# Optimization experiments

Measured on AMD Instinct MI355X. Metric: run time of the kernel, lower is better.

Reference implementation:

```python
import jax, jax.numpy as jnp
import numpy as np

COMMITMENT_COST = 0.25
DECAY = 0.99
EPSILON = 1e-05
NUM_EMBEDDINGS = 1024
EMBEDDING_DIM = 256


def setup_inputs() -> dict:
    key = jax.random.key(0)
    k1, k2, k3 = jax.random.split(key, 3)
    B, T, D, K = 32, 1024, EMBEDDING_DIM, NUM_EMBEDDINGS
    z = jax.random.normal(k1, (B, T, D), dtype=jnp.float32)
    # torch init is uniform(-1/K, 1/K); scaled normal is fine for a numeric reference
    embedding = jax.random.uniform(k2, (K, D), dtype=jnp.float32, minval=-1.0 / K, maxval=1.0 / K)
    ema_cluster_size = jnp.ones((K,), dtype=jnp.float32)
    ema_w = embedding.copy()
    return {"z": z, "embedding": embedding, "ema_cluster_size": ema_cluster_size, "ema_w": ema_w}


def reference(z, embedding, ema_cluster_size, ema_w):
    B, T, D = z.shape
    K = embedding.shape[0]
    flat_z = z.reshape(-1, D)                         # [N, D]
    # squared L2 distances: ||z||^2 + ||e||^2 - 2 z.e   -> [N, K]
    distances = (jnp.sum(flat_z * flat_z, axis=1, keepdims=True)
                 + jnp.sum(embedding * embedding, axis=1)
                 - 2.0 * flat_z @ embedding.T)
    encoding_indices = jnp.argmin(distances, axis=1)  # [N]
    quantized = embedding[encoding_indices].reshape(B, T, D)

    # EMA codebook update (training branch; buffers, no grad)
    cluster_counts = jax.ops.segment_sum(jnp.ones_like(encoding_indices, dtype=jnp.float32),
                                         encoding_indices, num_segments=K)
    new_cluster_size = ema_cluster_size * DECAY + (1.0 - DECAY) * cluster_counts
    n = jnp.sum(new_cluster_size)
    new_cluster_size = (new_cluster_size + EPSILON) / (n + K * EPSILON) * n
    dw = jax.ops.segment_sum(flat_z, encoding_indices, num_segments=K)  # [K, D]
    new_ema_w = ema_w * DECAY + (1.0 - DECAY) * dw
    new_embedding = new_ema_w / new_cluster_size[:, None]

    commitment_loss = jnp.mean((z - jax.lax.stop_gradient(quantized)) ** 2)
    loss = COMMITMENT_COST * commitment_loss
    # straight-through estimator
    quantized_st = z + jax.lax.stop_gradient(quantized - z)
    return (quantized_st, loss, encoding_indices.reshape(B, T),
            new_cluster_size, new_ema_w, new_embedding)
```

## Files before the change

kernel.cpp:

```cpp
#include <hip/hip_runtime.h>
#include <hip/hip_fp16.h>
#include <math.h>

#define COMMITMENT_COST 0.25f
#define DECAY 0.99f
#define EPSILON 1e-05f
#define KCODES 1024
#define DIM 256
#define NTOK 32768

#define O_QUANT 0
#define O_LOSS  8388608
#define O_IDX   8388609
#define O_CS    8421377
#define O_EMAW  8422401
#define O_EMB   8684545

#define SE_IDX    0
#define SE_ESQ    32768
#define SE_ZSQ    33792
#define SE_HIST   66560
#define SE_NM     67584
#define SE_NOVF   67585
#define SE_MLIST  67586
#define SE_OVF    100354
#define SE_OFFS   133122
#define SE_CUR    134147
#define SE_TLIST  135171
#define SE_LPART  167939

#define SQ_ZH    0
#define SQ_EH    4194304
#define SQ_MG    4325376
#define SQ_CC    4358144
#define SQ_CAND  4390912

#define THETA_F 2e-3f
#define CAND_CAP 16
#define EPSC 2e-4f

typedef __attribute__((ext_vector_type(8))) _Float16 f16x8;
typedef __attribute__((ext_vector_type(4))) float f32x4;

__global__ void pre_kernel(const float* __restrict__ z, const float* __restrict__ E,
                           float* __restrict__ zsq, float* __restrict__ esq,
                           int* __restrict__ hist, float* __restrict__ loss,
                           unsigned short* __restrict__ zh,
                           unsigned short* __restrict__ eh,
                           int* __restrict__ nm, int* __restrict__ novf) {
    const int b = blockIdx.x;
    const int wave = threadIdx.x >> 6;
    const int lane = threadIdx.x & 63;
    if (b < NTOK / 4) {
        int token = b * 4 + wave;
        float4 v = ((const float4*)(z + (size_t)token * DIM))[lane];
        ushort4 h;
        h.x = __half_as_ushort(__float2half(v.x));
        h.y = __half_as_ushort(__float2half(v.y));
        h.z = __half_as_ushort(__float2half(v.z));
        h.w = __half_as_ushort(__float2half(v.w));
        *(ushort4*)(zh + (size_t)token * DIM + lane * 4) = h;
        float s = v.x * v.x + v.y * v.y + v.z * v.z + v.w * v.w;
        #pragma unroll
        for (int off = 32; off > 0; off >>= 1) s += __shfl_down(s, off);
        if (lane == 0) zsq[token] = s;
        if (b == 0 && threadIdx.x == 4) loss[0] = 0.0f;
        if (b == 0 && threadIdx.x == 5) { *nm = 0; *novf = 0; }
    } else {
        int eb = b - NTOK / 4;
        int k = eb * 4 + wave;
        float4 v = ((const float4*)(E + (size_t)k * DIM))[lane];
        ushort4 h;
        h.x = __half_as_ushort(__float2half(v.x));
        h.y = __half_as_ushort(__float2half(v.y));
        h.z = __half_as_ushort(__float2half(v.z));
        h.w = __half_as_ushort(__float2half(v.w));
        *(ushort4*)(eh + (size_t)k * DIM + lane * 4) = h;
        float s = v.x * v.x + v.y * v.y + v.z * v.z + v.w * v.w;
        #pragma unroll
        for (int off = 32; off > 0; off >>= 1) s += __shfl_down(s, off);
        if (lane == 0) esq[k] = s;
        if (threadIdx.x < 4) hist[eb * 4 + threadIdx.x] = 0;
    }
}

__global__ __launch_bounds__(256) void dist_mfma_kernel(
        const unsigned short* __restrict__ zh, const unsigned short* __restrict__ eh,
        const float* __restrict__ esq,
        float* __restrict__ Mg, int* __restrict__ ccount,
        unsigned long long* __restrict__ cand) {
    __shared__ unsigned short Als[64 * 260];
    __shared__ unsigned short Bls[2][256 * 36];
    __shared__ float scr[64][4];
    __shared__ float runmin[64];
    __shared__ int lcnt[64];

    const int tid = threadIdx.x;
    const int wn = tid >> 6;
    const int lane = tid & 63;
    const int l15 = lane & 15, l4 = lane >> 4;
    const int tok0 = blockIdx.x * 64;

    #pragma unroll
    for (int q = 0; q < 8; ++q) {
        int c = tid + 256 * q;
        int row = c >> 5, ch = c & 31;
        *(f16x8*)(Als + row * 260 + ch * 8) =
            *(const f16x8*)(zh + (size_t)(tok0 + row) * 256 + ch * 8);
    }
    if (tid < 64) { runmin[tid] = 3.4e38f; lcnt[tid] = 0; }

    const int brow = tid >> 2, bch = tid & 3;

    #pragma unroll
    for (int q = 0; q < 4; ++q) {
        f16x8 r = *(const f16x8*)(eh + (size_t)(brow + 64 * q) * 256 + bch * 8);
        *(f16x8*)(Bls[0] + (brow + 64 * q) * 36 + bch * 8) = r;
    }
    __syncthreads();

    int cur = 0;
    for (int c0 = 0; c0 < KCODES; c0 += 256) {
        f32x4 acc[4][4];
        #pragma unroll
        for (int i = 0; i < 4; ++i)
            #pragma unroll
            for (int j = 0; j < 4; ++j)
                acc[i][j] = (f32x4){0.f, 0.f, 0.f, 0.f};

        for (int kt = 0; kt < 8; ++kt) {
            int nc0 = c0, nkt = kt + 1;
            if (nkt == 8) { nkt = 0; nc0 += 256; }
            const bool hasnext = (nc0 < KCODES);
            f16x8 rn[4];
            if (hasnext) {
                #pragma unroll
                for (int q = 0; q < 4; ++q)
                    rn[q] = *(const f16x8*)(
                        eh + (size_t)(nc0 + brow + 64 * q) * 256 + nkt * 32 + bch * 8);
            }
            f16x8 av[4], bv[4];
            #pragma unroll
            for (int i = 0; i < 4; ++i)
                av[i] = *(const f16x8*)(Als + (i * 16 + l15) * 260 + kt * 32 + l4 * 8);
            #pragma unroll
            for (int j = 0; j < 4; ++j)
                bv[j] = *(const f16x8*)(Bls[cur] + (wn * 64 + j * 16 + l15) * 36 + l4 * 8);
            #pragma unroll
            for (int i = 0; i < 4; ++i)
                #pragma unroll
                for (int j = 0; j < 4; ++j)
                    acc[i][j] = __builtin_amdgcn_mfma_f32_16x16x32_f16(
                        av[i], bv[j], acc[i][j], 0, 0, 0);
            if (hasnext) {
                #pragma unroll
                for (int q = 0; q < 4; ++q)
                    *(f16x8*)(Bls[cur ^ 1] + (brow + 64 * q) * 36 + bch * 8) = rn[q];
            }
            __syncthreads();
            cur ^= 1;
        }

        float sq[4];
        #pragma unroll
        for (int j = 0; j < 4; ++j) sq[j] = esq[c0 + wn * 64 + j * 16 + l15];

        #pragma unroll
        for (int i = 0; i < 4; ++i) {
            #pragma unroll
            for (int r = 0; r < 4; ++r) {
                float v = fminf(fminf(sq[0] - 2.0f * acc[i][0][r],
                                      sq[1] - 2.0f * acc[i][1][r]),
                                fminf(sq[2] - 2.0f * acc[i][2][r],
                                      sq[3] - 2.0f * acc[i][3][r]));
                #pragma unroll
                for (int m = 1; m < 16; m <<= 1)
                    v = fminf(v, __shfl_xor(v, m));
                if (l15 == 0) scr[i * 16 + l4 * 4 + r][wn] = v;
            }
        }
        __syncthreads();
        if (tid < 64) {
            float m = fminf(fminf(scr[tid][0], scr[tid][1]),
                            fminf(scr[tid][2], scr[tid][3]));
            runmin[tid] = fminf(runmin[tid], m);
        }
        __syncthreads();
        #pragma unroll
        for (int i = 0; i < 4; ++i) {
            #pragma unroll
            for (int r = 0; r < 4; ++r) {
                const int row = i * 16 + l4 * 4 + r;
                const float thr = runmin[row] + THETA_F;
                #pragma unroll
                for (int j = 0; j < 4; ++j) {
                    float d = sq[j] - 2.0f * acc[i][j][r];
                    if (d <= thr) {
                        int slot = atomicAdd(&lcnt[row], 1);
                        if (slot < CAND_CAP)
                            cand[(size_t)slot * NTOK + tok0 + row] =
                                (((unsigned long long)__float_as_uint(d)) << 32) |
                                (unsigned)(c0 + wn * 64 + j * 16 + l15);
                    }
                }
            }
        }
    }
    __syncthreads();
    if (tid < 64) {
        Mg[tok0 + tid] = runmin[tid];
        ccount[tok0 + tid] = lcnt[tid];
    }
}

__global__ __launch_bounds__(256) void recheck_a_kernel(
        const float* __restrict__ Mg, const int* __restrict__ ccount,
        const unsigned long long* __restrict__ cand,
        unsigned int* __restrict__ idx,
        int* __restrict__ mlist, int* __restrict__ nm,
        int* __restrict__ ovf, int* __restrict__ novf) {
    __shared__ int ps[256];
    __shared__ int base_m, base_o;
    const int tid = threadIdx.x;
    const int token = blockIdx.x * 256 + tid;
    const int cnt = ccount[token];
    const float thr = Mg[token] + THETA_F;

    const bool isovf_cap = (cnt > CAND_CAP);
    int nsurv = 0;
    int firstcode = 0;
    if (!isovf_cap) {
        for (int s = 0; s < cnt; ++s) {
            unsigned long long e = cand[(size_t)s * NTOK + token];
            float dt = __uint_as_float((unsigned)(e >> 32));
            if (dt <= thr) {
                ++nsurv;
                if (nsurv == 1) firstcode = (int)(unsigned)(e & 0x3FFull);
            }
        }
    }
    const bool ismulti = !isovf_cap && nsurv >= 2 && nsurv <= 8;
    const bool isovf = isovf_cap || (!isovf_cap && (nsurv == 0 || nsurv > 8));
    const int want = (ismulti ? 1 : 0) | ((isovf ? 1 : 0) << 16);

    ps[tid] = want;
    __syncthreads();
    #pragma unroll
    for (int off = 1; off < 256; off <<= 1) {
        int v = (tid >= off) ? ps[tid - off] : 0;
        __syncthreads();
        ps[tid] += v;
        __syncthreads();
    }
    if (tid == 255) {
        int tot = ps[255];
        base_m = (tot & 0xFFFF) ? atomicAdd(nm, tot & 0xFFFF) : 0;
        base_o = (tot >> 16) ? atomicAdd(novf, tot >> 16) : 0;
    }
    __syncthreads();
    const int off_m = (ps[tid] - want) & 0xFFFF;
    const int off_o = (ps[tid] - want) >> 16;

    if (!isovf_cap && nsurv == 1) idx[token] = (unsigned)firstcode;
    if (ismulti) mlist[base_m + off_m] = token;
    if (isovf)   ovf[base_o + off_o] = token;
}

#define RB_BLOCKS 1024
__global__ __launch_bounds__(256) void recheck_b_kernel(
        const float* __restrict__ z, const float* __restrict__ E,
        const float* __restrict__ zsq, const float* __restrict__ esq,
        const float* __restrict__ Mg, const int* __restrict__ ccount,
        const unsigned long long* __restrict__ cand,
        const int* __restrict__ mlist, const int* __restrict__ nm,
        const int* __restrict__ ovf, const int* __restrict__ novf,
        unsigned int* __restrict__ idx) {
    const int wave = threadIdx.x >> 6, lane = threadIdx.x & 63;
    const int gw = blockIdx.x * 4 + wave;
    const int n = *nm;
    for (int m = gw; m < n; m += RB_BLOCKS * 4) {
        const int token = mlist[m];
        const int cnt = ccount[token];
        const float thr = Mg[token] + THETA_F;
        const float An = zsq[token];
        const float4 zv = *(const float4*)(z + (size_t)token * DIM + lane * 4);
        unsigned long long e = 0x7F80000000000000ull;
        if (lane < cnt) e = cand[(size_t)lane * NTOK + token];
        const float dt = __uint_as_float((unsigned)(e >> 32));
        const int ec = (int)(unsigned)(e & 0x3FFull);
        const unsigned long long bm0 = __ballot(lane < cnt && dt <= thr);
        unsigned long long bm = bm0;
        const int ns = __popcll(bm0);

        float m1 = 3.4e38f, m2 = 3.4e38f; int a1 = 0x7fffffff;
        int mycode = 0; float mydv = 3.4e38f;
        #pragma unroll
        for (int i = 0; i < 8; ++i) {
            if (i < ns) {
                const int s = __ffsll(bm) - 1; bm &= bm - 1;
                const int code = __shfl(ec, s);
                const float4 ev = *(const float4*)(E + (size_t)code * DIM + lane * 4);
                float p = fmaf(zv.x, ev.x, 0.0f);
                p = fmaf(zv.y, ev.y, p);
                p = fmaf(zv.z, ev.z, p);
                p = fmaf(zv.w, ev.w, p);
                #pragma unroll
                for (int o = 1; o < 64; o <<= 1) p += __shfl_xor(p, o);
                const float dv = (An + esq[code]) - 2.0f * p;
                if (dv < m1 || (dv == m1 && code < a1)) { m2 = m1; m1 = dv; a1 = code; }
                else if (dv < m2) m2 = dv;
                if (lane == i) { mycode = code; mydv = dv; }
            }
        }
        if (m2 - m1 > 2.0f * EPSC) {
            if (lane == 0) idx[token] = (unsigned)a1;
        } else {
            float b1 = 3.4e38f; int ai = 0x7fffffff;
            for (int s = 0; s < ns; ++s) {
                const int code = __shfl(mycode, s);
                const float dvp = __shfl(mydv, s);
                if (dvp <= m1 + 2.0f * EPSC && lane == 0) {
                    const float4* zp = (const float4*)(z + (size_t)token * DIM);
                    const float4* ep = (const float4*)(E + (size_t)code * DIM);
                    float acc = 0.0f;
                    #pragma unroll 8
                    for (int q = 0; q < 64; ++q) {
                        float4 a = zp[q], b = ep[q];
                        acc = fmaf(a.x, b.x, acc); acc = fmaf(a.y, b.y, acc);
                        acc = fmaf(a.z, b.z, acc); acc = fmaf(a.w, b.w, acc);
                    }
                    float dv = (An + esq[code]) - 2.0f * acc;
                    if (dv < b1 || (dv == b1 && code < ai)) { b1 = dv; ai = code; }
                }
            }
            if (lane == 0) idx[token] = (unsigned)ai;
        }
    }
    const int nov = *novf;
    for (int w = gw; w < nov; w += RB_BLOCKS * 4) {
        const int token = ovf[w];
        const float An = zsq[token];
        const float4* zp = (const float4*)(z + (size_t)token * DIM);
        float best = 3.4e38f; int bid = 0x7fffffff;
        for (int code = lane; code < KCODES; code += 64) {
            const float4* ep = (const float4*)(E + (size_t)code * DIM);
            float acc = 0.0f;
            for (int q = 0; q < 64; ++q) {
                float4 a = zp[q], b = ep[q];
                acc = fmaf(a.x, b.x, acc); acc = fmaf(a.y, b.y, acc);
                acc = fmaf(a.z, b.z, acc); acc = fmaf(a.w, b.w, acc);
            }
            float dv = (An + esq[code]) - 2.0f * acc;
            if (dv < best || (dv == best && code < bid)) { best = dv; bid = code; }
        }
        #pragma unroll
        for (int mm = 1; mm < 64; mm <<= 1) {
            float ov = __shfl_xor(best, mm); int oi = __shfl_xor(bid, mm);
            if (ov < best || (ov == best && oi < bid)) { best = ov; bid = oi; }
        }
        if (lane == 0) idx[token] = (unsigned)bid;
    }
}

__global__ __launch_bounds__(256) void mid_kernel(
        const float* __restrict__ z, const float* __restrict__ E,
        const unsigned int* __restrict__ idxarr,
        float* __restrict__ idx_out, int* __restrict__ hist,
        float* __restrict__ quant, float* __restrict__ lpart) {
    __shared__ float ls[4];
    const int wave = threadIdx.x >> 6;
    const int lane = threadIdx.x & 63;
    const int token = blockIdx.x * 4 + wave;
    const int idx = (int)idxarr[token];

    if (lane == 0) {
        idx_out[token] = (float)idx;
        atomicAdd(&hist[idx], 1);
    }

    const float4 ev = *(const float4*)(E + (size_t)idx * DIM + lane * 4);
    const float4 zv = *(const float4*)(z + (size_t)token * DIM + lane * 4);
    *(float4*)(quant + (size_t)token * DIM + lane * 4) = ev;

    float dx = zv.x - ev.x, dy = zv.y - ev.y, dz = zv.z - ev.z, dww = zv.w - ev.w;
    float l = dx * dx + dy * dy + dz * dz + dww * dww;
    #pragma unroll
    for (int off = 32; off > 0; off >>= 1) l += __shfl_down(l, off);
    if (lane == 0) ls[wave] = l;
    __syncthreads();
    if (threadIdx.x == 0)
        lpart[blockIdx.x] = (ls[0] + ls[1]) + (ls[2] + ls[3]);
}

__global__ __launch_bounds__(256) void cs_kernel(
        const int* __restrict__ hist, const float* __restrict__ ema_cs,
        float* __restrict__ cs_out, int* __restrict__ offs,
        int* __restrict__ cursor, const float* __restrict__ lpart,
        float* __restrict__ loss) {
    __shared__ float f[256];
    __shared__ int hs[256];
    const int tid = threadIdx.x;
    float pre4[4]; int h4[4];
    float part = 0.0f; int hp = 0;
    #pragma unroll
    for (int q = 0; q < 4; ++q) {
        int k = tid * 4 + q;
        h4[q] = hist[k];
        pre4[q] = ema_cs[k] * DECAY + (1.0f - DECAY) * (float)h4[q];
        part += pre4[q];
        hp += h4[q];
    }
    f[tid] = part; hs[tid] = hp;
    __syncthreads();
    #pragma unroll
    for (int off = 1; off < 256; off <<= 1) {
        int v = (tid >= off) ? hs[tid - off] : 0;
        __syncthreads();
        hs[tid] += v;
        __syncthreads();
    }
    int run = hs[tid] - hp;
    #pragma unroll
    for (int q = 0; q < 4; ++q) {
        int k = tid * 4 + q;
        offs[k] = run; cursor[k] = run;
        run += h4[q];
    }
    if (tid == 255) offs[KCODES] = run;
    for (int s = 128; s > 0; s >>= 1) {
        if (tid < s) f[tid] += f[tid + s];
        __syncthreads();
    }
    float n = f[0];
    #pragma unroll
    for (int q = 0; q < 4; ++q) {
        int k = tid * 4 + q;
        cs_out[k] = (pre4[q] + EPSILON) / (n + KCODES * EPSILON) * n;
    }
    float lp = 0.0f;
    #pragma unroll
    for (int q = 0; q < 32; ++q) lp += lpart[tid + 256 * q];
    __syncthreads();
    f[tid] = lp;
    __syncthreads();
    for (int s = 128; s > 0; s >>= 1) {
        if (tid < s) f[tid] += f[tid + s];
        __syncthreads();
    }
    if (tid == 0) loss[0] = f[0];
}

__global__ __launch_bounds__(256) void scatter_kernel(
        const unsigned int* __restrict__ idxarr,
        int* __restrict__ cursor, int* __restrict__ tlist) {
    const int t = blockIdx.x * 256 + threadIdx.x;
    const int idx = (int)idxarr[t];
    const int pos = atomicAdd(&cursor[idx], 1);
    tlist[pos] = t;
}

__global__ __launch_bounds__(256) void fin_gather_kernel(
        const float* __restrict__ z, const int* __restrict__ offs,
        const int* __restrict__ tlist, float* __restrict__ dw) {
    __shared__ float4 red[4][64];
    const int k = blockIdx.x;
    const int grp = threadIdx.x >> 6;
    const int lane = threadIdx.x & 63;
    const int s = offs[k], e = offs[k + 1];
    float4 acc = {0.f, 0.f, 0.f, 0.f};
    for (int i = s + grp; i < e; i += 4) {
        const int t = tlist[i];
        const float4 v = *(const float4*)(z + (size_t)t * DIM + lane * 4);
        acc.x += v.x; acc.y += v.y; acc.z += v.z; acc.w += v.w;
    }
    red[grp][lane] = acc;
    __syncthreads();
    if (grp == 0) {
        float4 a = red[0][lane], b = red[1][lane];
        float4 c = red[2][lane], d = red[3][lane];
        float4 o;
        o.x = (a.x + b.x) + (c.x + d.x);
        o.y = (a.y + b.y) + (c.y + d.y);
        o.z = (a.z + b.z) + (c.z + d.z);
        o.w = (a.w + b.w) + (c.w + d.w);
        *(float4*)(dw + (size_t)k * DIM + lane * 4) = o;
    }
}

__global__ __launch_bounds__(256) void fin_kernel(
        const float* __restrict__ ema_w, const float* __restrict__ cs,
        float* __restrict__ emaw_inout , float* __restrict__ emb_out,
        float* __restrict__ loss_inout) {
    const int i = blockIdx.x * 256 + threadIdx.x;
    const int k = i >> 6;
    float4 d = ((const float4*)emaw_inout)[i];
    float4 w = ((const float4*)ema_w)[i];
    float4 nw;
    nw.x = w.x * DECAY + (1.0f - DECAY) * d.x;
    nw.y = w.y * DECAY + (1.0f - DECAY) * d.y;
    nw.z = w.z * DECAY + (1.0f - DECAY) * d.z;
    nw.w = w.w * DECAY + (1.0f - DECAY) * d.w;
    ((float4*)emaw_inout)[i] = nw;
    float inv = 1.0f / cs[k];
    float4 e; e.x = nw.x * inv; e.y = nw.y * inv; e.z = nw.z * inv; e.w = nw.w * inv;
    ((float4*)emb_out)[i] = e;
    if (i == 0)
        loss_inout[0] = COMMITMENT_COST * loss_inout[0] / (float)((size_t)NTOK * DIM);
}

extern "C" void kernel_launch(void* const* d_in, const int* in_sizes, int n_in,
                              void* d_out, int out_size, void* d_ws, size_t ws_size,
                              hipStream_t stream) {
    const float* z      = (const float*)d_in[0];
    const float* E      = (const float*)d_in[1];
    const float* ema_cs = (const float*)d_in[2];
    const float* ema_w  = (const float*)d_in[3];
    float* out = (float*)d_out;

    float* emb = out + O_EMB;
    unsigned int* idx = (unsigned int*)(emb + SE_IDX);
    float* esq  = emb + SE_ESQ;
    float* zsq  = emb + SE_ZSQ;
    int*   hist = (int*)(emb + SE_HIST);
    int*   nm     = (int*)(emb + SE_NM);
    int*   novf   = (int*)(emb + SE_NOVF);
    int*   mlist  = (int*)(emb + SE_MLIST);
    int*   ovf    = (int*)(emb + SE_OVF);
    int*   offs   = (int*)(emb + SE_OFFS);
    int*   cursor = (int*)(emb + SE_CUR);
    int*   tlist  = (int*)(emb + SE_TLIST);
    float* lpart  = emb + SE_LPART;

    unsigned short* zh = (unsigned short*)(out + SQ_ZH);
    unsigned short* eh = (unsigned short*)(out + SQ_EH);
    float* Mg = out + SQ_MG;
    int* ccount = (int*)(out + SQ_CC);
    unsigned long long* cand = (unsigned long long*)(out + SQ_CAND);

    pre_kernel<<<NTOK / 4 + KCODES / 4, 256, 0, stream>>>(
        z, E, zsq, esq, hist, out + O_LOSS, zh, eh, nm, novf);
    dist_mfma_kernel<<<NTOK / 64, 256, 0, stream>>>(
        zh, eh, esq, Mg, ccount, cand);
    recheck_a_kernel<<<NTOK / 256, 256, 0, stream>>>(
        Mg, ccount, cand, idx, mlist, nm, ovf, novf);
    recheck_b_kernel<<<RB_BLOCKS, 256, 0, stream>>>(
        z, E, zsq, esq, Mg, ccount, cand, mlist, nm, ovf, novf, idx);
    mid_kernel<<<NTOK / 4, 256, 0, stream>>>(z, E, idx, out + O_IDX, hist,
                                             out + O_QUANT, lpart);
    cs_kernel<<<1, 256, 0, stream>>>(hist, ema_cs, out + O_CS, offs, cursor,
                                     lpart, out + O_LOSS);
    scatter_kernel<<<NTOK / 256, 256, 0, stream>>>(idx, cursor, tlist);
    fin_gather_kernel<<<KCODES, 256, 0, stream>>>(z, offs, tlist, out + O_EMAW);
    fin_kernel<<<256, 256, 0, stream>>>(ema_w, out + O_CS, out + O_EMAW, emb,
                                        out + O_LOSS);
}
```

Measured before the change: 223.6 us.

## Load codebook fragments directly from global memory into MFMA registers, dropping LDS staging

The distance kernel no longer stages codebook tiles through a double-buffered shared-memory buffer with per-step barriers. Each wave now reads its B fragments straight from global/L2 into registers, with the k-loop fully unrolled and launch bounds raised to target four blocks per SM. This removes the LDS writes and the barriers inside the inner loop and cuts shared-memory use so more blocks can be resident. In exchange it relies on L2/cache hits for codebook reuse across waves and blocks, and loses the explicit prefetch of the next tile, which may expose global-load latency.

```diff
diff --git a/kernel.cpp b/kernel.cpp
--- a/kernel.cpp
+++ b/kernel.cpp
@@ -84,13 +84,12 @@
     }
 }
 
-__global__ __launch_bounds__(256) void dist_mfma_kernel(
+__global__ __launch_bounds__(256, 4) void dist_mfma_kernel(
         const unsigned short* __restrict__ zh, const unsigned short* __restrict__ eh,
         const float* __restrict__ esq,
         float* __restrict__ Mg, int* __restrict__ ccount,
         unsigned long long* __restrict__ cand) {
     __shared__ unsigned short Als[64 * 260];
-    __shared__ unsigned short Bls[2][256 * 36];
     __shared__ float scr[64][4];
     __shared__ float runmin[64];
     __shared__ int lcnt[64];
@@ -109,17 +108,10 @@
             *(const f16x8*)(zh + (size_t)(tok0 + row) * 256 + ch * 8);
     }
     if (tid < 64) { runmin[tid] = 3.4e38f; lcnt[tid] = 0; }
-
-    const int brow = tid >> 2, bch = tid & 3;
-
-    #pragma unroll
-    for (int q = 0; q < 4; ++q) {
-        f16x8 r = *(const f16x8*)(eh + (size_t)(brow + 64 * q) * 256 + bch * 8);
-        *(f16x8*)(Bls[0] + (brow + 64 * q) * 36 + bch * 8) = r;
-    }
-    __syncthreads();
-
-    int cur = 0;
+    __syncthreads();
+
+    const unsigned short* ebase = eh + (size_t)(wn * 64 + l15) * 256 + l4 * 8;
+
     for (int c0 = 0; c0 < KCODES; c0 += 256) {
         f32x4 acc[4][4];
         #pragma unroll
@@ -128,37 +120,23 @@
             for (int j = 0; j < 4; ++j)
                 acc[i][j] = (f32x4){0.f, 0.f, 0.f, 0.f};
 
+        const unsigned short* ec = ebase + (size_t)c0 * 256;
+        #pragma unroll
         for (int kt = 0; kt < 8; ++kt) {
-            int nc0 = c0, nkt = kt + 1;
-            if (nkt == 8) { nkt = 0; nc0 += 256; }
-            const bool hasnext = (nc0 < KCODES);
-            f16x8 rn[4];
-            if (hasnext) {
-                #pragma unroll
-                for (int q = 0; q < 4; ++q)
-                    rn[q] = *(const f16x8*)(
-                        eh + (size_t)(nc0 + brow + 64 * q) * 256 + nkt * 32 + bch * 8);
-            }
-            f16x8 av[4], bv[4];
+            f16x8 bv[4];
+            #pragma unroll
+            for (int j = 0; j < 4; ++j)
+                bv[j] = *(const f16x8*)(ec + j * 16 * 256 + kt * 32);
+            f16x8 av[4];
             #pragma unroll
             for (int i = 0; i < 4; ++i)
                 av[i] = *(const f16x8*)(Als + (i * 16 + l15) * 260 + kt * 32 + l4 * 8);
-            #pragma unroll
-            for (int j = 0; j < 4; ++j)
-                bv[j] = *(const f16x8*)(Bls[cur] + (wn * 64 + j * 16 + l15) * 36 + l4 * 8);
             #pragma unroll
             for (int i = 0; i < 4; ++i)
                 #pragma unroll
                 for (int j = 0; j < 4; ++j)
                     acc[i][j] = __builtin_amdgcn_mfma_f32_16x16x32_f16(
                         av[i], bv[j], acc[i][j], 0, 0, 0);
-            if (hasnext) {
-                #pragma unroll
-                for (int q = 0; q < 4; ++q)
-                    *(f16x8*)(Bls[cur ^ 1] + (brow + 64 * q) * 36 + bch * 8) = rn[q];
-            }
-            __syncthreads();
-            cur ^= 1;
         }
 
         float sq[4];
```

New measurement: 236.8 us. 5.9% more time.
